# Kernel tuning notes

Measured on AMD Instinct MI355X. Metric: run time of the kernel, lower is better.

## Reference

```python
import jax, jax.numpy as jnp
import numpy as np

B, T, E, D = 8, 2048, 1024, 64  # batch, seq_len, n_emb, head_dim

def setup_inputs() -> dict:
    key = jax.random.key(0)
    ks = jax.random.split(key, 4)
    scale = 1.0 / np.sqrt(E)
    return {
        "x": jax.random.normal(ks[0], (B, T, E), dtype=jnp.float32),
        "Wq": jax.random.normal(ks[1], (E, D), dtype=jnp.float32) * scale,
        "bq": jnp.zeros((D,), dtype=jnp.float32),
        "Wk": jax.random.normal(ks[2], (E, D), dtype=jnp.float32) * scale,
        "bk": jnp.zeros((D,), dtype=jnp.float32),
        "Wv": jax.random.normal(ks[3], (E, D), dtype=jnp.float32) * scale,
        "bv": jnp.zeros((D,), dtype=jnp.float32),
    }

def reference(x, Wq, bq, Wk, bk, Wv, bv):
    # QKV projections: [B,T,E] @ [E,D] -> [B,T,D]
    q = x @ Wq + bq
    k = x @ Wk + bk
    v = x @ Wv + bv
    d = q.shape[-1]
    # scaled dot-product scores [B,T,T]
    wei = jnp.einsum('btd,bsd->bts', q, k) * (d ** -0.5)
    # causal mask: position t attends to s <= t
    t = wei.shape[1]
    causal = jnp.tril(jnp.ones((t, t), dtype=bool))
    wei = jnp.where(causal, wei, -jnp.inf)
    wei = jax.nn.softmax(wei, axis=-1)
    # attention output [B,T,D]
    return jnp.einsum('bts,bsd->btd', wei, v)
```

## Files before the change

kernel.cpp:

```cpp
#include <hip/hip_runtime.h>
#include <math.h>


#define B_   8
#define T_   2048
#define E_   1024
#define D_   64
#define BT_  (B_ * T_)

typedef __attribute__((ext_vector_type(8))) short s16x8;
typedef __attribute__((ext_vector_type(4))) short s16x4;
typedef __attribute__((ext_vector_type(4))) float f32x4;

__device__ __forceinline__ short f2bf(float f) {
    union { float f; unsigned u; } a; a.f = f;
    unsigned r = a.u + 0x7fffu + ((a.u >> 16) & 1u);
    return (short)(r >> 16);
}

#define MFMA16(a, b, c) __builtin_amdgcn_mfma_f32_16x16x32_bf16((a), (b), (c), 0, 0, 0)

#define DPPF(x, ctrl) __builtin_bit_cast(float, \
    __builtin_amdgcn_update_dpp(0, __builtin_bit_cast(int, (x)), (ctrl), 0xF, 0xF, true))

__device__ __forceinline__ float rsum16(float x) {
    x += DPPF(x, 0xB1);
    x += DPPF(x, 0x4E);
    x += DPPF(x, 0x124);
    x += DPPF(x, 0x128);
    return x;
}

__global__ __launch_bounds__(256) void wtrans_kernel(
    const float* __restrict__ Wq, const float* __restrict__ Wk,
    const float* __restrict__ Wv, short* __restrict__ Wt)
{
    __shared__ float sT[64][65];
    const int sel = blockIdx.x >> 4;
    const int k0  = (blockIdx.x & 15) * 64;
    const float* W = sel == 0 ? Wq : (sel == 1 ? Wk : Wv);
    const int t  = threadIdx.x;
    const int kr = t >> 4, c4 = (t & 15) * 4;
    #pragma unroll
    for (int i = 0; i < 4; ++i) {
        float4 v = *(const float4*)&W[(size_t)(k0 + kr + i * 16) * D_ + c4];
        sT[kr + i * 16][c4 + 0] = v.x; sT[kr + i * 16][c4 + 1] = v.y;
        sT[kr + i * 16][c4 + 2] = v.z; sT[kr + i * 16][c4 + 3] = v.w;
    }
    __syncthreads();
    #pragma unroll
    for (int i = 0; i < 4; ++i) {
        int n  = (t >> 4) + i * 16;
        int kk = (t & 15) * 4;
        s16x4 o;
        o.x = f2bf(sT[kk + 0][n]); o.y = f2bf(sT[kk + 1][n]);
        o.z = f2bf(sT[kk + 2][n]); o.w = f2bf(sT[kk + 3][n]);
        *(s16x4*)&Wt[(size_t)(sel * 64 + n) * E_ + k0 + kk] = o;
    }
}

__global__ __launch_bounds__(256) void qkv_kernel(
    const float* __restrict__ x, const short* __restrict__ Wt,
    const float* __restrict__ bq, const float* __restrict__ bk,
    const float* __restrict__ bv,
    short* __restrict__ Qg, short* __restrict__ Kg, short* __restrict__ VTg)
{
    __shared__ short sX[2][32 * 136];
    const int tid  = threadIdx.x;
    const int lane = tid & 63;
    const int w    = tid >> 6;
    const int l15  = lane & 15, quad = lane >> 4;
    const int t0   = blockIdx.x * 32;
    const int bb   = t0 >> 11;

    const int srow = tid >> 3;
    const int skc  = (tid & 7) * 16;
    const float* px = &x[(size_t)(t0 + srow) * E_ + skc];

    f32x4 acc[3][2];
    #pragma unroll
    for (int a = 0; a < 3; ++a)
        #pragma unroll
        for (int h = 0; h < 2; ++h)
            acc[a][h] = (f32x4){0.f, 0.f, 0.f, 0.f};

    float4 ld[4];
    #pragma unroll
    for (int i = 0; i < 4; ++i)
        ld[i] = *(const float4*)(px + i * 4);

    int buf = 0;
    for (int k0 = 0; k0 < E_; k0 += 128) {
        s16x8 pk0, pk1;
        pk0[0] = f2bf(ld[0].x); pk0[1] = f2bf(ld[0].y);
        pk0[2] = f2bf(ld[0].z); pk0[3] = f2bf(ld[0].w);
        pk0[4] = f2bf(ld[1].x); pk0[5] = f2bf(ld[1].y);
        pk0[6] = f2bf(ld[1].z); pk0[7] = f2bf(ld[1].w);
        pk1[0] = f2bf(ld[2].x); pk1[1] = f2bf(ld[2].y);
        pk1[2] = f2bf(ld[2].z); pk1[3] = f2bf(ld[2].w);
        pk1[4] = f2bf(ld[3].x); pk1[5] = f2bf(ld[3].y);
        pk1[6] = f2bf(ld[3].z); pk1[7] = f2bf(ld[3].w);
        *(s16x8*)&sX[buf][srow * 136 + skc]     = pk0;
        *(s16x8*)&sX[buf][srow * 136 + skc + 8] = pk1;
        __syncthreads();

        if (k0 + 128 < E_) {
            const float* p2 = px + k0 + 128;
            #pragma unroll
            for (int i = 0; i < 4; ++i)
                ld[i] = *(const float4*)(p2 + i * 4);
        }

        s16x8 aw[3][4];
        #pragma unroll
        for (int t3 = 0; t3 < 3; ++t3) {
            const short* pw = &Wt[(size_t)((w * 3 + t3) * 16 + l15) * E_ + k0 + quad * 8];
            #pragma unroll
            for (int c = 0; c < 4; ++c)
                aw[t3][c] = *(const s16x8*)(pw + 32 * c);
        }
        s16x8 bxf[2][4];
        #pragma unroll
        for (int h = 0; h < 2; ++h)
            #pragma unroll
            for (int c = 0; c < 4; ++c)
                bxf[h][c] = *(const s16x8*)&sX[buf][(h * 16 + l15) * 136 + 32 * c + quad * 8];
        #pragma unroll
        for (int t3 = 0; t3 < 3; ++t3)
            #pragma unroll
            for (int h = 0; h < 2; ++h)
                #pragma unroll
                for (int c = 0; c < 4; ++c)
                    acc[t3][h] = MFMA16(aw[t3][c], bxf[h][c], acc[t3][h]);
        buf ^= 1;
    }

    __syncthreads();
    short* sVT = &sX[0][0];

    #pragma unroll
    for (int t3 = 0; t3 < 3; ++t3) {
        const int nt = w * 3 + t3;
        const int fb = (nt & 3) * 16 + quad * 4;
        const float* bias = nt < 4 ? bq : (nt < 8 ? bk : bv);
        f32x4 bsv = *(const f32x4*)&bias[fb];
        #pragma unroll
        for (int h = 0; h < 2; ++h) {
            const int tok = t0 + h * 16 + l15;
            f32x4 v = acc[t3][h] + bsv;
            if (nt < 4) {
                v *= 0.125f;
                s16x4 o = { f2bf(v[0]), f2bf(v[1]), f2bf(v[2]), f2bf(v[3]) };
                *(s16x4*)&Qg[(size_t)tok * D_ + fb] = o;
            } else if (nt < 8) {
                s16x4 o = { f2bf(v[0]), f2bf(v[1]), f2bf(v[2]), f2bf(v[3]) };
                *(s16x4*)&Kg[(size_t)tok * D_ + fb] = o;
            } else {
                const int lt = h * 16 + l15;
                #pragma unroll
                for (int r = 0; r < 4; ++r)
                    sVT[(fb + r) * 48 + lt] = f2bf(v[r]);
            }
        }
    }
    __syncthreads();
    {
        const int d  = tid >> 2;
        const int tq = (tid & 3) * 8;
        s16x8 vv = *(const s16x8*)&sVT[d * 48 + tq];
        *(s16x8*)&VTg[(size_t)(bb * D_ + d) * T_ + (t0 & (T_ - 1)) + tq] = vv;
    }
}

__global__ __launch_bounds__(256) void attn_kernel(
    const short* __restrict__ Qg, const short* __restrict__ Kg,
    const short* __restrict__ VTg, float* __restrict__ out)
{
    __shared__ char smem[20736];
    short* sP = (short*)smem;
    float* sO = (float*)smem;
    float* sl = (float*)(smem + 20480);

    const int tid  = threadIdx.x;
    const int lane = tid & 63;
    const int w    = tid >> 6;
    const int l15  = lane & 15, quad = lane >> 4;
    const int b    = blockIdx.x & 7;
    const int j    = 127 - (blockIdx.x >> 3);
    const int tq0  = j * 16;
    const int nch  = (j >> 2) + 1;
    const int seg  = (nch + 3) >> 2;
    const int c0   = w * seg;
    const int c1   = (c0 + seg < nch) ? c0 + seg : nch;

    const size_t qoff = ((size_t)b * T_ + tq0 + l15) * D_ + quad * 8;
    const s16x8 aq0 = *(const s16x8*)&Qg[qoff];
    const s16x8 aq1 = *(const s16x8*)&Qg[qoff + 32];

    f32x4 oacc[4];
    float lpart[4] = {0.f, 0.f, 0.f, 0.f};
    #pragma unroll
    for (int nt = 0; nt < 4; ++nt) oacc[nt] = (f32x4){0.f, 0.f, 0.f, 0.f};

    const short* kb = Kg  + (size_t)b * T_ * D_;
    const short* vb = VTg + (size_t)b * D_ * T_;
    short* sPw = sP + w * (16 * 72);

    for (int c = c0; c < c1; ++c) {
        const int s0 = c * 64;

        s16x8 bk[4][2];
        #pragma unroll
        for (int nt = 0; nt < 4; ++nt) {
            const short* pk = kb + (size_t)(s0 + nt * 16 + l15) * D_ + quad * 8;
            bk[nt][0] = *(const s16x8*)pk;
            bk[nt][1] = *(const s16x8*)(pk + 32);
        }
        const f32x4 zz = (f32x4){0.f, 0.f, 0.f, 0.f};
        f32x4 sacc[4];
        #pragma unroll
        for (int nt = 0; nt < 4; ++nt) {
            sacc[nt] = MFMA16(aq0, bk[nt][0], zz);
            sacc[nt] = MFMA16(aq1, bk[nt][1], sacc[nt]);
        }

        s16x8 bv[4][2];
        #pragma unroll
        for (int nt = 0; nt < 4; ++nt) {
            const short* pv = vb + (size_t)(nt * 16 + l15) * T_ + s0 + quad * 8;
            bv[nt][0] = *(const s16x8*)pv;
            bv[nt][1] = *(const s16x8*)(pv + 32);
        }

        const bool diag = (c == nch - 1);
        float p[4][4];
        #pragma unroll
        for (int nt = 0; nt < 4; ++nt)
            #pragma unroll
            for (int r = 0; r < 4; ++r) {
                float e = __expf(sacc[nt][r]);
                if (diag && (s0 + nt * 16 + l15 > tq0 + quad * 4 + r)) e = 0.f;
                p[nt][r] = e;
            }
        #pragma unroll
        for (int r = 0; r < 4; ++r)
            lpart[r] += (p[0][r] + p[1][r]) + (p[2][r] + p[3][r]);

        #pragma unroll
        for (int nt = 0; nt < 4; ++nt)
            #pragma unroll
            for (int r = 0; r < 4; ++r)
                sPw[(quad * 4 + r) * 72 + nt * 16 + l15] = f2bf(p[nt][r]);
        s16x8 ap0 = *(const s16x8*)&sPw[l15 * 72 + quad * 8];
        s16x8 ap1 = *(const s16x8*)&sPw[l15 * 72 + 32 + quad * 8];

        #pragma unroll
        for (int nt = 0; nt < 4; ++nt) {
            oacc[nt] = MFMA16(ap0, bv[nt][0], oacc[nt]);
            oacc[nt] = MFMA16(ap1, bv[nt][1], oacc[nt]);
        }
    }

    f32x4 lv;
    #pragma unroll
    for (int r = 0; r < 4; ++r) lv[r] = rsum16(lpart[r]);

    __syncthreads();
    float* sOw = sO + w * (64 * 20);
    #pragma unroll
    for (int nt = 0; nt < 4; ++nt)
        *(f32x4*)&sOw[(nt * 16 + l15) * 20 + quad * 4] = oacc[nt];
    if (l15 == 0)
        *(f32x4*)&sl[w * 16 + quad * 4] = lv;
    __syncthreads();

    const int d  = tid & 63;
    const int rb = (tid >> 6) * 4;
    f32x4 osum = (f32x4){0.f, 0.f, 0.f, 0.f};
    f32x4 lsum = (f32x4){0.f, 0.f, 0.f, 0.f};
    #pragma unroll
    for (int w2 = 0; w2 < 4; ++w2) {
        osum += *(const f32x4*)&sO[w2 * (64 * 20) + d * 20 + rb];
        lsum += *(const f32x4*)&sl[w2 * 16 + rb];
    }
    #pragma unroll
    for (int i = 0; i < 4; ++i)
        out[((size_t)b * T_ + tq0 + rb + i) * D_ + d] = osum[i] / lsum[i];
}

extern "C" void kernel_launch(void* const* d_in, const int* in_sizes, int n_in,
                              void* d_out, int out_size, void* d_ws, size_t ws_size,
                              hipStream_t stream) {
    (void)in_sizes; (void)n_in; (void)out_size; (void)ws_size;
    const float* x  = (const float*)d_in[0];
    const float* Wq = (const float*)d_in[1];
    const float* bq = (const float*)d_in[2];
    const float* Wk = (const float*)d_in[3];
    const float* bk = (const float*)d_in[4];
    const float* Wv = (const float*)d_in[5];
    const float* bv = (const float*)d_in[6];

    char* ws = (char*)d_ws;
    short* Qg  = (short*)(ws);
    short* Kg  = (short*)(ws + (size_t)2 * 1024 * 1024);
    short* VTg = (short*)(ws + (size_t)4 * 1024 * 1024);
    short* Wt  = (short*)(ws + (size_t)6 * 1024 * 1024);

    wtrans_kernel<<<48, 256, 0, stream>>>(Wq, Wk, Wv, Wt);
    qkv_kernel<<<BT_ / 32, 256, 0, stream>>>(x, Wt, bq, bk, bv, Qg, Kg, VTg);
    attn_kernel<<<B_ * 128, 256, 0, stream>>>(Qg, Kg, VTg, (float*)d_out);
}
```

Baseline: 165.1 us.

## Retile QKV projection to 64-token blocks and prefetch K/V in attention

The QKV projection now processes 64 tokens per block with a 64-wide k-step, and keeps two register stages of x loads in flight. This reuses each W fragment across four token subtiles instead of two, and the kernel drops the barrier before the V-transpose staging. The attention kernel double-buffers K and V fragments in registers, loading the next 64-key chunk while the current one is computed, and both kernels get occupancy hints. The cost is higher register pressure and only half as many QKV blocks, which may leave CUs underused.

Measured after the change: 180.8 us. 1.09x slower.

```diff
diff --git a/kernel.cpp b/kernel.cpp
--- a/kernel.cpp
+++ b/kernel.cpp
@@ -59,83 +59,80 @@
     }
 }
 
-__global__ __launch_bounds__(256) void qkv_kernel(
+__global__ __launch_bounds__(256, 2) void qkv_kernel(
     const float* __restrict__ x, const short* __restrict__ Wt,
     const float* __restrict__ bq, const float* __restrict__ bk,
     const float* __restrict__ bv,
     short* __restrict__ Qg, short* __restrict__ Kg, short* __restrict__ VTg)
 {
-    __shared__ short sX[2][32 * 136];
+    __shared__ short sX[2][64 * 72];
     const int tid  = threadIdx.x;
     const int lane = tid & 63;
     const int w    = tid >> 6;
     const int l15  = lane & 15, quad = lane >> 4;
-    const int t0   = blockIdx.x * 32;
+    const int t0   = blockIdx.x * 64;
     const int bb   = t0 >> 11;
 
-    const int srow = tid >> 3;
-    const int skc  = (tid & 7) * 16;
+    const int srow = tid >> 2;
+    const int skc  = (tid & 3) * 16;
     const float* px = &x[(size_t)(t0 + srow) * E_ + skc];
 
-    f32x4 acc[3][2];
+    f32x4 acc[3][4];
     #pragma unroll
     for (int a = 0; a < 3; ++a)
         #pragma unroll
-        for (int h = 0; h < 2; ++h)
+        for (int h = 0; h < 4; ++h)
             acc[a][h] = (f32x4){0.f, 0.f, 0.f, 0.f};
 
-    float4 ld[4];
-    #pragma unroll
-    for (int i = 0; i < 4; ++i)
-        ld[i] = *(const float4*)(px + i * 4);
+    float4 lda[4], ldb[4];
+    #pragma unroll
+    for (int i = 0; i < 4; ++i) lda[i] = *(const float4*)(px + i * 4);
+    #pragma unroll
+    for (int i = 0; i < 4; ++i) ldb[i] = *(const float4*)(px + 64 + i * 4);
 
     int buf = 0;
-    for (int k0 = 0; k0 < E_; k0 += 128) {
+    for (int k0 = 0; k0 < E_; k0 += 64) {
         s16x8 pk0, pk1;
-        pk0[0] = f2bf(ld[0].x); pk0[1] = f2bf(ld[0].y);
-        pk0[2] = f2bf(ld[0].z); pk0[3] = f2bf(ld[0].w);
-        pk0[4] = f2bf(ld[1].x); pk0[5] = f2bf(ld[1].y);
-        pk0[6] = f2bf(ld[1].z); pk0[7] = f2bf(ld[1].w);
-        pk1[0] = f2bf(ld[2].x); pk1[1] = f2bf(ld[2].y);
-        pk1[2] = f2bf(ld[2].z); pk1[3] = f2bf(ld[2].w);
-        pk1[4] = f2bf(ld[3].x); pk1[5] = f2bf(ld[3].y);
-        pk1[6] = f2bf(ld[3].z); pk1[7] = f2bf(ld[3].w);
-        *(s16x8*)&sX[buf][srow * 136 + skc]     = pk0;
-        *(s16x8*)&sX[buf][srow * 136 + skc + 8] = pk1;
+        pk0[0] = f2bf(lda[0].x); pk0[1] = f2bf(lda[0].y);
+        pk0[2] = f2bf(lda[0].z); pk0[3] = f2bf(lda[0].w);
+        pk0[4] = f2bf(lda[1].x); pk0[5] = f2bf(lda[1].y);
+        pk0[6] = f2bf(lda[1].z); pk0[7] = f2bf(lda[1].w);
+        pk1[0] = f2bf(lda[2].x); pk1[1] = f2bf(lda[2].y);
+        pk1[2] = f2bf(lda[2].z); pk1[3] = f2bf(lda[2].w);
+        pk1[4] = f2bf(lda[3].x); pk1[5] = f2bf(lda[3].y);
+        pk1[6] = f2bf(lda[3].z); pk1[7] = f2bf(lda[3].w);
+        *(s16x8*)&sX[buf][srow * 72 + skc]     = pk0;
+        *(s16x8*)&sX[buf][srow * 72 + skc + 8] = pk1;
         __syncthreads();
 
+        #pragma unroll
+        for (int i = 0; i < 4; ++i) lda[i] = ldb[i];
         if (k0 + 128 < E_) {
             const float* p2 = px + k0 + 128;
             #pragma unroll
-            for (int i = 0; i < 4; ++i)
-                ld[i] = *(const float4*)(p2 + i * 4);
-        }
-
-        s16x8 aw[3][4];
-        #pragma unroll
-        for (int t3 = 0; t3 < 3; ++t3) {
-            const short* pw = &Wt[(size_t)((w * 3 + t3) * 16 + l15) * E_ + k0 + quad * 8];
-            #pragma unroll
-            for (int c = 0; c < 4; ++c)
-                aw[t3][c] = *(const s16x8*)(pw + 32 * c);
-        }
-        s16x8 bxf[2][4];
-        #pragma unroll
-        for (int h = 0; h < 2; ++h)
-            #pragma unroll
-            for (int c = 0; c < 4; ++c)
-                bxf[h][c] = *(const s16x8*)&sX[buf][(h * 16 + l15) * 136 + 32 * c + quad * 8];
-        #pragma unroll
-        for (int t3 = 0; t3 < 3; ++t3)
-            #pragma unroll
-            for (int h = 0; h < 2; ++h)
+            for (int i = 0; i < 4; ++i) ldb[i] = *(const float4*)(p2 + i * 4);
+        }
+
+        #pragma unroll
+        for (int c = 0; c < 2; ++c) {
+            s16x8 aw[3];
+            #pragma unroll
+            for (int t3 = 0; t3 < 3; ++t3)
+                aw[t3] = *(const s16x8*)&Wt[(size_t)((w * 3 + t3) * 16 + l15) * E_
+                                            + k0 + c * 32 + quad * 8];
+            s16x8 bx[4];
+            #pragma unroll
+            for (int h = 0; h < 4; ++h)
+                bx[h] = *(const s16x8*)&sX[buf][(h * 16 + l15) * 72 + c * 32 + quad * 8];
+            #pragma unroll
+            for (int t3 = 0; t3 < 3; ++t3)
                 #pragma unroll
-                for (int c = 0; c < 4; ++c)
-                    acc[t3][h] = MFMA16(aw[t3][c], bxf[h][c], acc[t3][h]);
+                for (int h = 0; h < 4; ++h)
+                    acc[t3][h] = MFMA16(aw[t3], bx[h], acc[t3][h]);
+        }
         buf ^= 1;
     }
 
-    __syncthreads();
     short* sVT = &sX[0][0];
 
     #pragma unroll
@@ -145,7 +142,7 @@
         const float* bias = nt < 4 ? bq : (nt < 8 ? bk : bv);
         f32x4 bsv = *(const f32x4*)&bias[fb];
         #pragma unroll
-        for (int h = 0; h < 2; ++h) {
+        for (int h = 0; h < 4; ++h) {
             const int tok = t0 + h * 16 + l15;
             f32x4 v = acc[t3][h] + bsv;
             if (nt < 4) {
@@ -159,20 +156,23 @@
                 const int lt = h * 16 + l15;
                 #pragma unroll
                 for (int r = 0; r < 4; ++r)
-                    sVT[(fb + r) * 48 + lt] = f2bf(v[r]);
+                    sVT[(fb + r) * 72 + lt] = f2bf(v[r]);
             }
         }
     }
     __syncthreads();
     {
         const int d  = tid >> 2;
-        const int tq = (tid & 3) * 8;
-        s16x8 vv = *(const s16x8*)&sVT[d * 48 + tq];
-        *(s16x8*)&VTg[(size_t)(bb * D_ + d) * T_ + (t0 & (T_ - 1)) + tq] = vv;
-    }
-}
-
-__global__ __launch_bounds__(256) void attn_kernel(
+        const int tq = (tid & 3) * 16;
+        s16x8 v0 = *(const s16x8*)&sVT[d * 72 + tq];
+        s16x8 v1 = *(const s16x8*)&sVT[d * 72 + tq + 8];
+        short* pout = &VTg[(size_t)(bb * D_ + d) * T_ + (t0 & (T_ - 1)) + tq];
+        *(s16x8*)pout = v0;
+        *(s16x8*)(pout + 8) = v1;
+    }
+}
+
+__global__ __launch_bounds__(256, 4) void attn_kernel(
     const short* __restrict__ Qg, const short* __restrict__ Kg,
     const short* __restrict__ VTg, float* __restrict__ out)
 {
@@ -206,30 +206,39 @@
     const short* vb = VTg + (size_t)b * D_ * T_;
     short* sPw = sP + w * (16 * 72);
 
+    const int cini = (c0 < nch) ? c0 : nch - 1;
+    s16x8 bk[4][2], bv[4][2];
+    #pragma unroll
+    for (int nt = 0; nt < 4; ++nt) {
+        const short* pk = kb + (size_t)(cini * 64 + nt * 16 + l15) * D_ + quad * 8;
+        bk[nt][0] = *(const s16x8*)pk;
+        bk[nt][1] = *(const s16x8*)(pk + 32);
+        const short* pv = vb + (size_t)(nt * 16 + l15) * T_ + cini * 64 + quad * 8;
+        bv[nt][0] = *(const s16x8*)pv;
+        bv[nt][1] = *(const s16x8*)(pv + 32);
+    }
+
     for (int c = c0; c < c1; ++c) {
         const int s0 = c * 64;
-
-        s16x8 bk[4][2];
+        const int sn = (c + 1 < c1 ? c + 1 : c) * 64;
+
+        s16x8 nk[4][2], nv[4][2];
         #pragma unroll
         for (int nt = 0; nt < 4; ++nt) {
-            const short* pk = kb + (size_t)(s0 + nt * 16 + l15) * D_ + quad * 8;
-            bk[nt][0] = *(const s16x8*)pk;
-            bk[nt][1] = *(const s16x8*)(pk + 32);
-        }
+            const short* pk = kb + (size_t)(sn + nt * 16 + l15) * D_ + quad * 8;
+            nk[nt][0] = *(const s16x8*)pk;
+            nk[nt][1] = *(const s16x8*)(pk + 32);
+            const short* pv = vb + (size_t)(nt * 16 + l15) * T_ + sn + quad * 8;
+            nv[nt][0] = *(const s16x8*)pv;
+            nv[nt][1] = *(const s16x8*)(pv + 32);
+        }
+
         const f32x4 zz = (f32x4){0.f, 0.f, 0.f, 0.f};
         f32x4 sacc[4];
         #pragma unroll
         for (int nt = 0; nt < 4; ++nt) {
             sacc[nt] = MFMA16(aq0, bk[nt][0], zz);
             sacc[nt] = MFMA16(aq1, bk[nt][1], sacc[nt]);
-        }
-
-        s16x8 bv[4][2];
-        #pragma unroll
-        for (int nt = 0; nt < 4; ++nt) {
-            const short* pv = vb + (size_t)(nt * 16 + l15) * T_ + s0 + quad * 8;
-            bv[nt][0] = *(const s16x8*)pv;
-            bv[nt][1] = *(const s16x8*)(pv + 32);
         }
 
         const bool diag = (c == nch - 1);
@@ -258,6 +267,12 @@
         for (int nt = 0; nt < 4; ++nt) {
             oacc[nt] = MFMA16(ap0, bv[nt][0], oacc[nt]);
             oacc[nt] = MFMA16(ap1, bv[nt][1], oacc[nt]);
+        }
+
+        #pragma unroll
+        for (int nt = 0; nt < 4; ++nt) {
+            bk[nt][0] = nk[nt][0]; bk[nt][1] = nk[nt][1];
+            bv[nt][0] = nv[nt][0]; bv[nt][1] = nv[nt][1];
         }
     }
 
@@ -307,6 +322,6 @@
     short* Wt  = (short*)(ws + (size_t)6 * 1024 * 1024);
 
     wtrans_kernel<<<48, 256, 0, stream>>>(Wq, Wk, Wv, Wt);
-    qkv_kernel<<<BT_ / 32, 256, 0, stream>>>(x, Wt, bq, bk, bv, Qg, Kg, VTg);
+    qkv_kernel<<<BT_ / 64, 256, 0, stream>>>(x, Wt, bq, bk, bv, Qg, Kg, VTg);
     attn_kernel<<<B_ * 128, 256, 0, stream>>>(Qg, Kg, VTg, (float*)d_out);
 }
```
